# Kernel tuning notes

Hardware: AMD Instinct MI355X
Metric: run time of the kernel (lower is better)

The kernel has to match this reference:

```python
import jax, jax.numpy as jnp
import numpy as np

B, T, C = 2, 4096, 768
NH = 12
HD = C // NH  # 64


def setup_inputs() -> dict:
    key = jax.random.key(0)
    k0, k1, k2, k3, k4 = jax.random.split(key, 5)
    x = jax.random.normal(k0, (B, T, C), dtype=jnp.float32)
    # parameters (stored as [in, out] for x @ W)
    w_attn = jax.random.normal(k1, (C, 3 * C), dtype=jnp.float32) * 0.02
    b_attn = jnp.zeros((3 * C,), dtype=jnp.float32)
    w_proj = jax.random.normal(k2, (C, C), dtype=jnp.float32) * 0.02
    b_proj = jnp.zeros((C,), dtype=jnp.float32)
    return {"x": x, "w_attn": w_attn, "b_attn": b_attn, "w_proj": w_proj, "b_proj": b_proj}


def reference(x, w_attn, b_attn, w_proj, b_proj):
    Bv, Tv, Cv = x.shape
    qkv = x @ w_attn + b_attn  # (B,T,3C)
    q, k, v = jnp.split(qkv, 3, axis=2)
    # (B, NH, T, HD)
    q = q.reshape(Bv, Tv, NH, HD).transpose(0, 2, 1, 3)
    k = k.reshape(Bv, Tv, NH, HD).transpose(0, 2, 1, 3)
    v = v.reshape(Bv, Tv, NH, HD).transpose(0, 2, 1, 3)
    att = jnp.einsum('bhqd,bhkd->bhqk', q, k) / jnp.sqrt(jnp.float32(HD))
    causal = jnp.tril(jnp.ones((Tv, Tv), dtype=bool))  # mask buffer slice
    att = jnp.where(causal[None, None, :, :], att, jnp.float32(-jnp.inf))
    att = jax.nn.softmax(att, axis=-1)
    y = jnp.einsum('bhqk,bhkd->bhqd', att, v)
    y = y.transpose(0, 2, 1, 3).reshape(Bv, Tv, Cv)
    y = y @ w_proj + b_proj
    return y
```

## Files before the change

kernel.cpp:

```cpp
#include <hip/hip_runtime.h>

typedef __bf16 bf16;
typedef float f32x4 __attribute__((ext_vector_type(4)));
typedef bf16 bf16x8v __attribute__((ext_vector_type(8)));
typedef bf16 bf16x4v __attribute__((ext_vector_type(4)));

#define MFMA_BF16(a, b, c) __builtin_amdgcn_mfma_f32_16x16x32_bf16((a), (b), (c), 0, 0, 0)

__device__ __forceinline__ void async16(const bf16* g, bf16* l) {
  __builtin_amdgcn_global_load_lds(
      (const __attribute__((address_space(1))) void*)g,
      (__attribute__((address_space(3))) void*)l, 16, 0, 0);
}

__global__ __launch_bounds__(256) void prep_kernel(
    const float* __restrict__ x, bf16* __restrict__ xb,
    const float* __restrict__ w_attn, bf16* __restrict__ wt_attn,
    const float* __restrict__ w_proj, bf16* __restrict__ wt_proj) {
  __shared__ float tile[32][33];
  const int b = blockIdx.x;
  if (b < 3072) {
    int i = b * 256 + threadIdx.x;
    const float4* p = (const float4*)x + (size_t)i * 2;
    float4 a = p[0], c = p[1];
    bf16x8v o;
    o[0] = (bf16)a.x; o[1] = (bf16)a.y; o[2] = (bf16)a.z; o[3] = (bf16)a.w;
    o[4] = (bf16)c.x; o[5] = (bf16)c.y; o[6] = (bf16)c.z; o[7] = (bf16)c.w;
    ((bf16x8v*)xb)[i] = o;
    return;
  }
  const float* in;
  bf16* out;
  int Ccols, bidx;
  if (b < 4800) {
    in = w_attn; out = wt_attn; Ccols = 2304; bidx = b - 3072;
  } else {
    in = w_proj; out = wt_proj; Ccols = 768; bidx = b - 4800;
  }
  const int R = 768;
  const int gx = Ccols / 32;
  const int c0 = (bidx % gx) * 32, r0 = (bidx / gx) * 32;
  const int tx = threadIdx.x & 31;
  const int ty = threadIdx.x >> 5;
#pragma unroll
  for (int i = 0; i < 4; ++i) {
    int r = ty + i * 8;
    tile[r][tx] = in[(size_t)(r0 + r) * Ccols + c0 + tx];
  }
  __syncthreads();
#pragma unroll
  for (int i = 0; i < 4; ++i) {
    int c = ty + i * 8;
    out[(size_t)(c0 + c) * R + r0 + tx] = (bf16)tile[tx][c];
  }
}

__global__ __launch_bounds__(256) void transpose_bf16_kernel(
    const bf16* __restrict__ in, bf16* __restrict__ out, int R, int Ccols) {
  __shared__ bf16 tile[32][33];
  const bf16* inp = in + (size_t)blockIdx.z * R * Ccols;
  bf16* outp = out + (size_t)blockIdx.z * R * Ccols;
  int c0 = blockIdx.x * 32, r0 = blockIdx.y * 32;
  int tx = threadIdx.x & 31;
  int ty = threadIdx.x >> 5;
#pragma unroll
  for (int i = 0; i < 4; ++i) {
    int r = ty + i * 8;
    tile[r][tx] = inp[(size_t)(r0 + r) * Ccols + c0 + tx];
  }
  __syncthreads();
#pragma unroll
  for (int i = 0; i < 4; ++i) {
    int c = ty + i * 8;
    outp[(size_t)(c0 + c) * R + r0 + tx] = tile[tx][c];
  }
}

template <int MODE, int BM, int BN>
__global__ __launch_bounds__(256, 3) void gemm_kernel(
    const bf16* __restrict__ A, const bf16* __restrict__ Bt,
    const float* __restrict__ bias, int N, float* __restrict__ outf,
    bf16* __restrict__ qo, bf16* __restrict__ ko, bf16* __restrict__ vo) {
  constexpr int Kdim = 768;
  constexpr int MI = BM / 32;
  constexpr int NI = BN / 32;
  constexpr int TPX = (8192 / BM) / 8;
  __shared__ __align__(16) bf16 As[BM][64];
  __shared__ __align__(16) bf16 Bs[BN][64];
  const int tid = threadIdx.x;
  const int lane = tid & 63;
  const int wave = tid >> 6;
  const int wm = (wave >> 1) * (BM / 2), wn = (wave & 1) * (BN / 2);
  const int id = blockIdx.x;
  const int xcd = id & 7, j = id >> 3;
  const int m0 = (xcd * TPX + j % TPX) * BM;
  const int n0 = (j / TPX) * BN;
  const int l15 = lane & 15, q4 = lane >> 4;
  const int swz = l15 & 7;

  f32x4 acc[MI][NI] = {};

  const int gr = lane >> 3;
  const int sj = (lane & 7) ^ gr;

  for (int k0 = 0; k0 < Kdim; k0 += 64) {
#pragma unroll
    for (int c = 0; c < BM / 32; ++c) {
      const int r0 = wave * (BM / 4) + c * 8;
      async16(A + (size_t)(m0 + r0 + gr) * Kdim + k0 + sj * 8, &As[r0][0]);
    }
#pragma unroll
    for (int c = 0; c < BN / 32; ++c) {
      const int r0 = wave * (BN / 4) + c * 8;
      async16(Bt + (size_t)(n0 + r0 + gr) * Kdim + k0 + sj * 8, &Bs[r0][0]);
    }
    __syncthreads();
#pragma unroll
    for (int ks = 0; ks < 2; ++ks) {
      bf16x8v af[MI], bfg[NI];
#pragma unroll
      for (int i = 0; i < MI; ++i)
        af[i] =
            *(const bf16x8v*)&As[wm + i * 16 + l15][((ks * 4 + q4) ^ swz) * 8];
#pragma unroll
      for (int i = 0; i < NI; ++i)
        bfg[i] =
            *(const bf16x8v*)&Bs[wn + i * 16 + l15][((ks * 4 + q4) ^ swz) * 8];
#pragma unroll
      for (int mi = 0; mi < MI; ++mi)
#pragma unroll
        for (int ni = 0; ni < NI; ++ni)
          acc[mi][ni] = MFMA_BF16(af[mi], bfg[ni], acc[mi][ni]);
    }
    __syncthreads();
  }

#pragma unroll
  for (int mi = 0; mi < MI; ++mi) {
#pragma unroll
    for (int ni = 0; ni < NI; ++ni) {
      int col = n0 + wn + ni * 16 + l15;
      float bv = bias[col];
#pragma unroll
      for (int r = 0; r < 4; ++r) {
        int row = m0 + wm + mi * 16 + q4 * 4 + r;
        float val = acc[mi][ni][r] + bv;
        if (MODE == 0) {
          outf[(size_t)row * N + col] = val;
        } else {
          int sel = col / 768;
          int cc = col - sel * 768;
          int h = cc >> 6, d = cc & 63;
          int b = row >> 12, t = row & 4095;
          bf16* dst = sel == 0 ? qo : (sel == 1 ? ko : vo);
          dst[((size_t)(b * 12 + h) * 4096 + t) * 64 + d] = (bf16)val;
        }
      }
    }
  }
}

__global__ __launch_bounds__(512, 6) void attn_kernel(
    const bf16* __restrict__ q, const bf16* __restrict__ k,
    const bf16* __restrict__ vt, bf16* __restrict__ y) {
  __shared__ __align__(16) bf16 Kb[2][64][64];
  __shared__ __align__(16) bf16 Vb[2][64][64];
  __shared__ __align__(16) bf16 Ps[8][16][64];
  const int tid = threadIdx.x;
  const int lane = tid & 63, wave = tid >> 6;
  const int l15 = lane & 15, q4 = lane >> 4;
  const int swz = l15 & 7;
  const int id = blockIdx.x;
  const int bh = id % 24;
  const int p = id / 24;
  const int rs = (wave < 4) ? ((63 - p) * 64 + wave * 16)
                            : (p * 64 + (wave - 4) * 16);
  const int hb = bh % 12, bb = bh / 12;

  const int gr = lane >> 3;
  const int sj = (lane & 7) ^ gr;
  const bf16* kgbase = k + (size_t)bh * 4096 * 64;
  const bf16* vgbase = vt + (size_t)bh * 64 * 4096;

  bf16x8v ones;
#pragma unroll
  for (int j = 0; j < 8; ++j) ones[j] = (bf16)1.0f;

  bf16x8v qf[2];
  {
    const bf16* qrow = q + ((size_t)bh * 4096 + rs + l15) * 64 + q4 * 8;
#pragma unroll
    for (int ks = 0; ks < 2; ++ks) {
      bf16x8v t8 = *(const bf16x8v*)(qrow + ks * 32);
#pragma unroll
      for (int j = 0; j < 8; ++j) t8[j] = (bf16)((float)t8[j] * 0.18033688f);
      qf[ks] = t8;
    }
  }

  f32x4 o[4] = {};
  f32x4 ol = {};

  auto stage = [&](int kt, int buf) {
    const int t0k = kt * 64;
    async16(kgbase + (size_t)(t0k + wave * 8 + gr) * 64 + sj * 8,
            &Kb[buf][wave * 8][0]);
    async16(vgbase + (size_t)(wave * 8 + gr) * 4096 + t0k + sj * 8,
            &Vb[buf][wave * 8][0]);
  };

  auto sm_full = [&](f32x4 (&s)[4]) {
#pragma unroll
    for (int ni = 0; ni < 4; ++ni)
#pragma unroll
      for (int r = 0; r < 4; ++r)
        s[ni][r] = __builtin_amdgcn_exp2f(s[ni][r] - 28.8539008f);
  };
  auto sm_mask = [&](f32x4 (&s)[4], int lim) {
#pragma unroll
    for (int ni = 0; ni < 4; ++ni)
#pragma unroll
      for (int r = 0; r < 4; ++r)
        s[ni][r] = (ni * 16 + q4 * 4 + r <= lim)
                       ? __builtin_amdgcn_exp2f(s[ni][r] - 28.8539008f)
                       : 0.0f;
  };
  auto pwrite = [&](const f32x4 (&s)[4]) {
#pragma unroll
    for (int ni = 0; ni < 4; ++ni) {
      bf16x4v pv4;
#pragma unroll
      for (int e = 0; e < 4; ++e) pv4[e] = (bf16)s[ni][e];
      const int jb = ni * 2 + (q4 >> 1);
      *(bf16x4v*)&Ps[wave][l15][((jb ^ (l15 & 7)) * 8) + (q4 & 1) * 4] = pv4;
    }
  };

  const int ktmax = 64 - p;
  stage(0, 0);

  for (int kt = 0; kt < ktmax; ++kt) {
    const int buf = kt & 1;
    __syncthreads();
    if (kt + 1 < ktmax) stage(kt + 1, buf ^ 1);
    const int t0 = kt * 64;

    if (t0 <= rs + 15) {
      f32x4 s[4] = {};
      __builtin_amdgcn_s_setprio(1);
#pragma unroll
      for (int ni = 0; ni < 4; ++ni) {
#pragma unroll
        for (int ks = 0; ks < 2; ++ks) {
          bf16x8v kf = *(const bf16x8v*)&Kb[buf][ni * 16 + l15]
                                           [((ks * 4 + q4) ^ swz) * 8];
          s[ni] = MFMA_BF16(kf, qf[ks], s[ni]);
        }
      }
      __builtin_amdgcn_s_setprio(0);

      if (t0 + 63 <= rs) sm_full(s); else sm_mask(s, rs + l15 - t0);
      pwrite(s);

      bf16x8v pf[2];
#pragma unroll
      for (int ks = 0; ks < 2; ++ks)
        pf[ks] = *(const bf16x8v*)&Ps[wave][l15][((ks * 4 + q4) ^ swz) * 8];

      __builtin_amdgcn_s_setprio(1);
#pragma unroll
      for (int d4 = 0; d4 < 4; ++d4) {
#pragma unroll
        for (int ks = 0; ks < 2; ++ks) {
          bf16x8v vf = *(const bf16x8v*)&Vb[buf][d4 * 16 + l15]
                                           [((ks * 4 + q4) ^ swz) * 8];
          o[d4] = MFMA_BF16(pf[ks], vf, o[d4]);
        }
      }
#pragma unroll
      for (int ks = 0; ks < 2; ++ks) ol = MFMA_BF16(pf[ks], ones, ol);
      __builtin_amdgcn_s_setprio(0);
    }
  }

#pragma unroll
  for (int d4 = 0; d4 < 4; ++d4)
#pragma unroll
    for (int r = 0; r < 4; ++r) {
      int row = rs + q4 * 4 + r;
      y[((size_t)(bb * 4096 + row)) * 768 + hb * 64 + d4 * 16 + l15] =
          (bf16)(o[d4][r] / ol[r]);
    }
}

extern "C" void kernel_launch(void* const* d_in, const int* in_sizes, int n_in,
                              void* d_out, int out_size, void* d_ws,
                              size_t ws_size, hipStream_t stream) {
  const float* x = (const float*)d_in[0];
  const float* w_attn = (const float*)d_in[1];
  const float* b_attn = (const float*)d_in[2];
  const float* w_proj = (const float*)d_in[3];
  const float* b_proj = (const float*)d_in[4];
  float* out = (float*)d_out;

  char* ws = (char*)d_ws;
  size_t off = 0;
  auto carve = [&](size_t elems) {
    char* p = ws + off;
    off += ((elems * sizeof(bf16) + 255) & ~(size_t)255);
    return (bf16*)p;
  };
  bf16* xb = carve((size_t)8192 * 768);
  bf16* wt_attn = carve((size_t)2304 * 768);
  bf16* wt_proj = carve((size_t)768 * 768);
  bf16* qb = carve((size_t)24 * 4096 * 64);
  bf16* kb = carve((size_t)24 * 4096 * 64);
  bf16* vb = carve((size_t)24 * 4096 * 64);
  bf16* vtb = xb;
  bf16* yb = vb;

  prep_kernel<<<5376, 256, 0, stream>>>(x, xb, w_attn, wt_attn, w_proj,
                                        wt_proj);
  gemm_kernel<1, 128, 192><<<768, 256, 0, stream>>>(xb, wt_attn, b_attn, 2304,
                                                    nullptr, qb, kb, vb);
  transpose_bf16_kernel<<<dim3(64 / 32, 4096 / 32, 24), 256, 0, stream>>>(
      vb, vtb, 4096, 64);
  attn_kernel<<<dim3(768), 512, 0, stream>>>(qb, kb, vtb, yb);
  gemm_kernel<0, 64, 128><<<768, 256, 0, stream>>>(yb, wt_proj, b_proj, 768,
                                                   out, nullptr, nullptr,
                                                   nullptr);
}
```

Baseline: 219.1 us.

## Fuse V transpose into QKV GEMM epilogue via LDS staging

The QKV GEMM epilogue now handles V-column tiles by staging biased results in a swizzled LDS buffer, then writing V directly in transposed (d-major, t-contiguous) layout with 16-byte stores. This removes the separate transpose kernel launch and its extra global read and write of V. The transposed V lives in the output buffer until the final projection overwrites it. MODE 1 LDS grows to 48KB, which may lower occupancy for the QKV GEMM.

```diff
diff --git a/kernel.cpp b/kernel.cpp
--- a/kernel.cpp
+++ b/kernel.cpp
@@ -55,27 +55,6 @@
   }
 }
 
-__global__ __launch_bounds__(256) void transpose_bf16_kernel(
-    const bf16* __restrict__ in, bf16* __restrict__ out, int R, int Ccols) {
-  __shared__ bf16 tile[32][33];
-  const bf16* inp = in + (size_t)blockIdx.z * R * Ccols;
-  bf16* outp = out + (size_t)blockIdx.z * R * Ccols;
-  int c0 = blockIdx.x * 32, r0 = blockIdx.y * 32;
-  int tx = threadIdx.x & 31;
-  int ty = threadIdx.x >> 5;
-#pragma unroll
-  for (int i = 0; i < 4; ++i) {
-    int r = ty + i * 8;
-    tile[r][tx] = inp[(size_t)(r0 + r) * Ccols + c0 + tx];
-  }
-  __syncthreads();
-#pragma unroll
-  for (int i = 0; i < 4; ++i) {
-    int c = ty + i * 8;
-    outp[(size_t)(c0 + c) * R + r0 + tx] = tile[tx][c];
-  }
-}
-
 template <int MODE, int BM, int BN>
 __global__ __launch_bounds__(256, 3) void gemm_kernel(
     const bf16* __restrict__ A, const bf16* __restrict__ Bt,
@@ -85,8 +64,12 @@
   constexpr int MI = BM / 32;
   constexpr int NI = BN / 32;
   constexpr int TPX = (8192 / BM) / 8;
-  __shared__ __align__(16) bf16 As[BM][64];
-  __shared__ __align__(16) bf16 Bs[BN][64];
+  constexpr int BASE_E = (BM + BN) * 64;
+  constexpr int VT_E = 192 * 128;
+  constexpr int LDSE = (MODE == 1 && VT_E > BASE_E) ? VT_E : BASE_E;
+  __shared__ __align__(16) bf16 lds_all[LDSE];
+  bf16* asP = lds_all;
+  bf16* bsP = lds_all + BM * 64;
   const int tid = threadIdx.x;
   const int lane = tid & 63;
   const int wave = tid >> 6;
@@ -107,12 +90,12 @@
 #pragma unroll
     for (int c = 0; c < BM / 32; ++c) {
       const int r0 = wave * (BM / 4) + c * 8;
-      async16(A + (size_t)(m0 + r0 + gr) * Kdim + k0 + sj * 8, &As[r0][0]);
+      async16(A + (size_t)(m0 + r0 + gr) * Kdim + k0 + sj * 8, asP + r0 * 64);
     }
 #pragma unroll
     for (int c = 0; c < BN / 32; ++c) {
       const int r0 = wave * (BN / 4) + c * 8;
-      async16(Bt + (size_t)(n0 + r0 + gr) * Kdim + k0 + sj * 8, &Bs[r0][0]);
+      async16(Bt + (size_t)(n0 + r0 + gr) * Kdim + k0 + sj * 8, bsP + r0 * 64);
     }
     __syncthreads();
 #pragma unroll
@@ -120,12 +103,12 @@
       bf16x8v af[MI], bfg[NI];
 #pragma unroll
       for (int i = 0; i < MI; ++i)
-        af[i] =
-            *(const bf16x8v*)&As[wm + i * 16 + l15][((ks * 4 + q4) ^ swz) * 8];
+        af[i] = *(const bf16x8v*)(asP + (wm + i * 16 + l15) * 64 +
+                                  ((ks * 4 + q4) ^ swz) * 8);
 #pragma unroll
       for (int i = 0; i < NI; ++i)
-        bfg[i] =
-            *(const bf16x8v*)&Bs[wn + i * 16 + l15][((ks * 4 + q4) ^ swz) * 8];
+        bfg[i] = *(const bf16x8v*)(bsP + (wn + i * 16 + l15) * 64 +
+                                   ((ks * 4 + q4) ^ swz) * 8);
 #pragma unroll
       for (int mi = 0; mi < MI; ++mi)
 #pragma unroll
@@ -133,6 +116,42 @@
           acc[mi][ni] = MFMA_BF16(af[mi], bfg[ni], acc[mi][ni]);
     }
     __syncthreads();
+  }
+
+  if constexpr (MODE == 1) {
+    if (n0 >= 1536) {
+      bf16* vt = lds_all;
+#pragma unroll
+      for (int mi = 0; mi < MI; ++mi) {
+#pragma unroll
+        for (int ni = 0; ni < NI; ++ni) {
+          const int dl = wn + ni * 16 + l15;
+          const float bv = bias[n0 + dl];
+#pragma unroll
+          for (int r = 0; r < 4; ++r) {
+            const int tl = wm + mi * 16 + q4 * 4 + r;
+            vt[dl * 128 + (tl ^ ((dl & 15) << 3))] =
+                (bf16)(acc[mi][ni][r] + bv);
+          }
+        }
+      }
+      __syncthreads();
+      const int bb_ = m0 >> 12;
+      const int tblk = m0 & 4095;
+#pragma unroll
+      for (int i = 0; i < 12; ++i) {
+        const int lin = i * 256 + tid;
+        const int dl = lin >> 4;
+        const int p0 = (lin & 15) * 8;
+        const int tb = p0 ^ ((dl & 15) << 3);
+        bf16x8v v8 = *(const bf16x8v*)(vt + dl * 128 + p0);
+        const int cc = n0 + dl - 1536;
+        const int h = cc >> 6, dd = cc & 63;
+        *(bf16x8v*)&vo[(((size_t)(bb_ * 12 + h) * 64 + dd) * 4096) + tblk +
+                       tb] = v8;
+      }
+      return;
+    }
   }
 
 #pragma unroll
@@ -152,7 +171,7 @@
           int cc = col - sel * 768;
           int h = cc >> 6, d = cc & 63;
           int b = row >> 12, t = row & 4095;
-          bf16* dst = sel == 0 ? qo : (sel == 1 ? ko : vo);
+          bf16* dst = sel == 0 ? qo : ko;
           dst[((size_t)(b * 12 + h) * 4096 + t) * 64 + d] = (bf16)val;
         }
       }
@@ -316,15 +335,13 @@
   bf16* qb = carve((size_t)24 * 4096 * 64);
   bf16* kb = carve((size_t)24 * 4096 * 64);
   bf16* vb = carve((size_t)24 * 4096 * 64);
-  bf16* vtb = xb;
+  bf16* vtb = (bf16*)out;
   bf16* yb = vb;
 
   prep_kernel<<<5376, 256, 0, stream>>>(x, xb, w_attn, wt_attn, w_proj,
                                         wt_proj);
   gemm_kernel<1, 128, 192><<<768, 256, 0, stream>>>(xb, wt_attn, b_attn, 2304,
-                                                    nullptr, qb, kb, vb);
-  transpose_bf16_kernel<<<dim3(64 / 32, 4096 / 32, 24), 256, 0, stream>>>(
-      vb, vtb, 4096, 64);
+                                                    nullptr, qb, kb, vtb);
   attn_kernel<<<dim3(768), 512, 0, stream>>>(qb, kb, vtb, yb);
   gemm_kernel<0, 64, 128><<<768, 256, 0, stream>>>(yb, wt_proj, b_proj, 768,
                                                    out, nullptr, nullptr,
```

Result: faster. 213.1 us (-2.7%).
